# Kernel tuning notes

Hardware: AMD Instinct MI355X
Metric: run time of the kernel (lower is better)

## Reference

```python
import jax, jax.numpy as jnp
import numpy as np

T, C, NH, NL, NP = 5, 192, 4, 5, 4
DH = C // NH

def leaky(x):
    return jnp.where(x >= 0, x, 0.1 * x)

def conv2d(x, w, b, padding=1, dilation=1):
    out = jax.lax.conv_general_dilated(
        x, w, window_strides=(1, 1),
        padding=[(padding, padding), (padding, padding)],
        rhs_dilation=(dilation, dilation),
        dimension_numbers=('NCHW', 'OIHW', 'NCHW'))
    return out + b[None, :, None, None]

def grid_sample_border(img, gx, gy):
    # align_corners=True, padding_mode='border'; gx/gy normalized [-1,1], shape (B,H,W)
    B, Cc, H, W = img.shape
    x = jnp.clip((gx + 1.0) * 0.5 * (W - 1), 0.0, W - 1)
    y = jnp.clip((gy + 1.0) * 0.5 * (H - 1), 0.0, H - 1)
    x0 = jnp.floor(x); y0 = jnp.floor(y)
    wx = (x - x0).reshape(B, 1, -1); wy = (y - y0).reshape(B, 1, -1)
    flat = img.reshape(B, Cc, H * W)
    def g(yi, xi):
        xi = jnp.clip(xi, 0, W - 1).astype(jnp.int32)
        yi = jnp.clip(yi, 0, H - 1).astype(jnp.int32)
        return jnp.take_along_axis(flat, (yi * W + xi).reshape(B, 1, -1), axis=2)
    out = (g(y0, x0) * (1 - wx) * (1 - wy) + g(y0, x0 + 1) * wx * (1 - wy)
         + g(y0 + 1, x0) * (1 - wx) * wy + g(y0 + 1, x0 + 1) * wx * wy)
    return out.reshape(B, Cc, H, W)

def warp(x, flo):
    B, _, H, W = x.shape
    xx = jnp.arange(W, dtype=jnp.float32)[None, :] * jnp.ones((H, 1), jnp.float32)
    yy = jnp.arange(H, dtype=jnp.float32)[:, None] * jnp.ones((1, W), jnp.float32)
    gx = 2.0 * (xx[None] + flo[:, 0]) / max(W - 1, 1) - 1.0
    gy = 2.0 * (yy[None] + flo[:, 1]) / max(H - 1, 1) - 1.0
    return grid_sample_border(x, gx, gy)

def deform_sample(v_img, loc):
    # v_img (N,D,H,W); loc (N,Q,P,2) in [0,1]; bilinear, zeros padding, align_corners=False
    N, D, H, W = v_img.shape
    Q, P = loc.shape[1], loc.shape[2]
    x = loc[..., 0] * W - 0.5
    y = loc[..., 1] * H - 0.5
    x0 = jnp.floor(x); y0 = jnp.floor(y)
    wx = (x - x0).reshape(N, 1, -1); wy = (y - y0).reshape(N, 1, -1)
    flat = v_img.reshape(N, D, H * W)
    def g(yi, xi):
        valid = ((xi >= 0) & (xi <= W - 1) & (yi >= 0) & (yi <= H - 1)).astype(v_img.dtype)
        xi_c = jnp.clip(xi, 0, W - 1).astype(jnp.int32)
        yi_c = jnp.clip(yi, 0, H - 1).astype(jnp.int32)
        return jnp.take_along_axis(flat, (yi_c * W + xi_c).reshape(N, 1, -1), axis=2) * valid.reshape(N, 1, -1)
    out = (g(y0, x0) * (1 - wx) * (1 - wy) + g(y0, x0 + 1) * wx * (1 - wy)
         + g(y0 + 1, x0) * (1 - wx) * wy + g(y0 + 1, x0 + 1) * wx * wy)
    return out.reshape(N, D, Q, P)

def _forward(frame, srcframe, flow_forward, flow_backward,
             w_qk, b_qk, w_v, b_v, w_vproj, b_vproj, w_off, b_off,
             w_attn, b_attn, w_out, b_out, w_ff, b_ff,
             w_ffn1, b_ffn1, w_ffn2, b_ffn2):
    b, t, c, h, w = frame.shape
    ff01, ff12 = flow_forward[:, 0], flow_forward[:, 1]
    fb32, fb43 = flow_backward[:, 2], flow_backward[:, 3]
    ff02 = ff01 + warp(ff12, ff01)
    fb42 = fb43 + warp(fb32, fb43)
    warp02 = warp(frame[:, 0], ff02)
    warp12 = warp(frame[:, 1], ff12)
    warp32 = warp(frame[:, 3], fb32)
    warp42 = warp(frame[:, 4], fb42)
    qk_in = jnp.concatenate([warp02, warp12, frame[:, 2], warp32, warp42,
                             flow_forward.reshape(b, -1, h, w),
                             flow_backward.reshape(b, -1, h, w)], axis=1)
    queries = leaky(conv2d(qk_in, w_qk, b_qk)).reshape(b, t, c, h, w)
    value = leaky(conv2d(frame.reshape(b, t * c, h, w), w_v, b_v)).reshape(b, t, c, h, w)

    Lq = t * h * w
    q_tok = queries.transpose(0, 1, 3, 4, 2).reshape(b, Lq, c)
    v_tok = value.transpose(0, 1, 3, 4, 2).reshape(b, Lq, c)
    v_proj = (v_tok @ w_vproj.T + b_vproj).reshape(b, t, h * w, NH, DH)

    offs = (q_tok @ w_off.T + b_off).reshape(b, Lq, NH, NL, NP, 2)
    aw = (q_tok @ w_attn.T + b_attn).reshape(b, Lq, NH, NL * NP)
    aw = jax.nn.softmax(aw, axis=-1).reshape(b, Lq, NH, NL, NP)

    # reference points (all valid ratios are ones): ((x+0.5)/W, (y+0.5)/H)
    rx = (jnp.arange(w, dtype=frame.dtype) + 0.5) / w
    ry = (jnp.arange(h, dtype=frame.dtype) + 0.5) / h
    ref = jnp.stack(jnp.meshgrid(rx, ry, indexing='xy'), axis=-1).reshape(h * w, 2)
    ref = jnp.tile(ref, (t, 1))  # (Lq, 2)

    norm = jnp.array([w, h], dtype=frame.dtype)
    # flow-guided per-level displacement toward the center frame (level 2)
    zero = jnp.zeros_like(ff12)
    flows = jnp.stack([ff02, ff12, zero, fb32, fb42], axis=1)  # (b,NL,2,h,w)
    flow_norm = (flows / norm[None, None, :, None, None]).transpose(0, 1, 3, 4, 2).reshape(b, NL, h * w, 2)
    flow_norm = jnp.tile(flow_norm.transpose(0, 2, 1, 3), (1, t, 1, 1))  # (b,Lq,NL,2)

    loc = (ref[None, :, None, None, None, :]
           + offs / norm[None, None, None, None, None, :]
           + flow_norm[:, :, None, :, None, :])  # (b,Lq,NH,NL,NP,2)

    acc = jnp.zeros((b * NH, DH, Lq), dtype=frame.dtype)
    for l in range(NL):
        v_l = v_proj[:, l].transpose(0, 2, 3, 1).reshape(b * NH, DH, h, w)
        loc_l = loc[:, :, :, l].transpose(0, 2, 1, 3, 4).reshape(b * NH, Lq, NP, 2)
        samp = deform_sample(v_l, loc_l)  # (b*NH, DH, Lq, NP)
        w_l = aw[:, :, :, l].transpose(0, 2, 1, 3).reshape(b * NH, 1, Lq, NP)
        acc = acc + (samp * w_l).sum(-1)
    attn = acc.reshape(b, NH, DH, Lq).transpose(0, 3, 1, 2).reshape(b, Lq, c)
    attn = attn @ w_out.T + b_out

    out = attn.reshape(b, t, h, w, c).transpose(0, 1, 4, 2, 3).reshape(b * t, c, h, w)
    out = conv2d(out, w_ff, b_ff)
    out = out.reshape(b, t, c, h, w) + frame
    seq_in = jnp.concatenate([out.reshape(b * t, c, h, w), srcframe.reshape(b * t, c, h, w)], axis=1)
    ffn = conv2d(seq_in, w_ffn1, b_ffn1, padding=2, dilation=2)
    ffn = conv2d(leaky(ffn), w_ffn2, b_ffn2)
    out = out.reshape(b * t, c, h, w) + ffn
    return out.reshape(b, t, c, h, w)

def setup_inputs():
    key = jax.random.key(0)
    ks = jax.random.split(key, 16)
    B, H, W = 2, 64, 64
    s = 0.02
    d = {}
    d['frame'] = jax.random.normal(ks[0], (B, T, C, H, W), jnp.float32)
    d['srcframe'] = jax.random.normal(ks[1], (B, T, C, H, W), jnp.float32)
    d['flow_forward'] = jax.random.normal(ks[2], (B, 4, 2, H, W), jnp.float32)
    d['flow_backward'] = jax.random.normal(ks[3], (B, 4, 2, H, W), jnp.float32)
    cin_qk = T * C + 4 * (T - 1)
    d['w_qk'] = jax.random.normal(ks[4], (T * C, cin_qk, 3, 3), jnp.float32) * s
    d['b_qk'] = jnp.zeros((T * C,), jnp.float32)
    d['w_v'] = jax.random.normal(ks[5], (T * C, T * C, 3, 3), jnp.float32) * s
    d['b_v'] = jnp.zeros((T * C,), jnp.float32)
    d['w_vproj'] = jax.random.normal(ks[6], (C, C), jnp.float32) * s
    d['b_vproj'] = jnp.zeros((C,), jnp.float32)
    d['w_off'] = jax.random.normal(ks[7], (NH * NL * NP * 2, C), jnp.float32) * s
    d['b_off'] = jax.random.normal(ks[8], (NH * NL * NP * 2,), jnp.float32)
    d['w_attn'] = jax.random.normal(ks[9], (NH * NL * NP, C), jnp.float32) * s
    d['b_attn'] = jnp.zeros((NH * NL * NP,), jnp.float32)
    d['w_out'] = jax.random.normal(ks[10], (C, C), jnp.float32) * s
    d['b_out'] = jnp.zeros((C,), jnp.float32)
    d['w_ff'] = jax.random.normal(ks[11], (C, C, 3, 3), jnp.float32) * s
    d['b_ff'] = jnp.zeros((C,), jnp.float32)
    d['w_ffn1'] = jax.random.normal(ks[12], (C, 2 * C, 3, 3), jnp.float32) * s
    d['b_ffn1'] = jnp.zeros((C,), jnp.float32)
    d['w_ffn2'] = jax.random.normal(ks[13], (C, C, 3, 3), jnp.float32) * s
    d['b_ffn2'] = jnp.zeros((C,), jnp.float32)
    return d

def reference(frame, srcframe, flow_forward, flow_backward, w_qk, b_qk, w_v, b_v, w_vproj, b_vproj, w_off, b_off, w_attn, b_attn, w_out, b_out, w_ff, b_ff, w_ffn1, b_ffn1, w_ffn2, b_ffn2):
    out = _forward(frame, srcframe, flow_forward, flow_backward, w_qk, b_qk, w_v, b_v, w_vproj, b_vproj, w_off, b_off, w_attn, b_attn, w_out, b_out, w_ff, b_ff, w_ffn1, b_ffn1, w_ffn2, b_ffn2)
    return (out, srcframe)
```

## Files before the change

### kernel.cpp

```cpp
#include <hip/hip_runtime.h>


#define HWPX 4096
#define PPXN 4624
#define LQ   20480

typedef __attribute__((ext_vector_type(8))) short  short8;
typedef __attribute__((ext_vector_type(4))) short  short4v;
typedef __attribute__((ext_vector_type(4))) float  f32x4;

__device__ __forceinline__ unsigned short f2bf(float f) {
    unsigned u = __float_as_uint(f);
    unsigned r = (u + 0x7FFF + ((u >> 16) & 1)) >> 16;
    return (unsigned short)r;
}
__device__ __forceinline__ float bf2f(unsigned short s) {
    return __uint_as_float(((unsigned)s) << 16);
}

__device__ __forceinline__ void gl_lds16(const unsigned short* g, unsigned short* l) {
    __builtin_amdgcn_global_load_lds(
        (const __attribute__((address_space(1))) unsigned int*)g,
        (__attribute__((address_space(3))) unsigned int*)l, 16, 0, 0);
}

__device__ __forceinline__ float bsample(const float* __restrict__ p, float sx, float sy) {
    sx = fminf(fmaxf(sx, 0.f), 63.f);
    sy = fminf(fmaxf(sy, 0.f), 63.f);
    float x0 = floorf(sx), y0 = floorf(sy);
    int ix0 = (int)x0, iy0 = (int)y0;
    int ix1 = ix0 < 63 ? ix0 + 1 : 63;
    int iy1 = iy0 < 63 ? iy0 + 1 : 63;
    float wx = sx - x0, wy = sy - y0;
    float v00 = p[iy0*64+ix0], v01 = p[iy0*64+ix1];
    float v10 = p[iy1*64+ix0], v11 = p[iy1*64+ix1];
    return (v00*(1.f-wx) + v01*wx)*(1.f-wy) + (v10*(1.f-wx) + v11*wx)*wy;
}

__device__ void dev_flow(int i, const float* __restrict__ ff,
                         const float* __restrict__ fb, float* __restrict__ flows) {
    int b = i >> 12, pix = i & 4095;
    int x = pix & 63, y = pix >> 6;
    const float* ff01 = ff + (size_t)(b*4+0)*2*HWPX;
    const float* ff12 = ff + (size_t)(b*4+1)*2*HWPX;
    const float* fb32 = fb + (size_t)(b*4+2)*2*HWPX;
    const float* fb43 = fb + (size_t)(b*4+3)*2*HWPX;
    float* F = flows + (size_t)b*5*2*HWPX;
    float ax = ff01[pix], ay = ff01[HWPX+pix];
    float sx = bsample(ff12,      (float)x+ax, (float)y+ay);
    float sy = bsample(ff12+HWPX, (float)x+ax, (float)y+ay);
    F[0*2*HWPX + pix]        = ax + sx;
    F[0*2*HWPX + HWPX + pix] = ay + sy;
    F[1*2*HWPX + pix]        = ff12[pix];
    F[1*2*HWPX + HWPX + pix] = ff12[HWPX+pix];
    F[2*2*HWPX + pix]        = 0.f;
    F[2*2*HWPX + HWPX + pix] = 0.f;
    F[3*2*HWPX + pix]        = fb32[pix];
    F[3*2*HWPX + HWPX + pix] = fb32[HWPX+pix];
    float bx = fb43[pix], by = fb43[HWPX+pix];
    float tx = bsample(fb32,      (float)x+bx, (float)y+by);
    float ty = bsample(fb32+HWPX, (float)x+bx, (float)y+by);
    F[4*2*HWPX + pix]        = bx + tx;
    F[4*2*HWPX + HWPX + pix] = by + ty;
}

__device__ void dev_wT(const float* __restrict__ w, unsigned short* __restrict__ wT,
                       int CI, int NKB, int cotile, int kblk, int tid) {
    unsigned short* dst = wT + ((size_t)(cotile*NKB + kblk))*18432;
    #pragma unroll
    for (int it = 0; it < 9; ++it) {
        int idx = it*256 + tid;
        int tap = idx >> 8, sub = idx & 255;
        int cg = sub >> 6, co = sub & 63;
        int cog = cotile*64 + co;
        int ci0 = kblk*32 + cg*8;
        short8 v;
        #pragma unroll
        for (int j = 0; j < 8; ++j) {
            int ci = ci0 + j;
            v[j] = (ci < CI) ? (short)f2bf(w[((size_t)cog*CI + ci)*9 + tap]) : (short)0;
        }
        *(short8*)(dst + (size_t)idx*8) = v;
    }
}

__device__ void dev_wg(const float* __restrict__ w1, const float* __restrict__ w2,
                       unsigned short* __restrict__ wg, int co_split, int CO,
                       int cotile, int tid) {
    unsigned short* dst = wg + (size_t)cotile*12288;
    #pragma unroll
    for (int it = 0; it < 6; ++it) {
        int idx = it*256 + tid;
        int kblk = idx >> 8, sub = idx & 255;
        int cg = sub >> 6, co = sub & 63;
        int cog = cotile*64 + co;
        int ci0 = kblk*32 + cg*8;
        short8 v = {};
        if (cog < CO) {
            const float* row = (cog < co_split) ? w1 + (size_t)cog*192
                                                : w2 + (size_t)(cog - co_split)*192;
            #pragma unroll
            for (int j = 0; j < 8; ++j) v[j] = (short)f2bf(row[ci0 + j]);
        }
        *(short8*)(dst + (size_t)idx*8) = v;
    }
}

__global__ __launch_bounds__(256) void k_wprep(
    const float* __restrict__ flow_f, const float* __restrict__ flow_b,
    float* __restrict__ flows,
    const float* __restrict__ w_qk, unsigned short* __restrict__ wT_qk,
    const float* __restrict__ w_v,  unsigned short* __restrict__ wT_v,
    const float* __restrict__ w_ff, unsigned short* __restrict__ wT_ff,
    const float* __restrict__ w_f1, unsigned short* __restrict__ wT_f1,
    const float* __restrict__ w_f2, unsigned short* __restrict__ wT_f2,
    const float* __restrict__ w_vp, const float* __restrict__ w_off,
    const float* __restrict__ w_at, const float* __restrict__ w_out,
    unsigned short* __restrict__ wg_vp, unsigned short* __restrict__ wg_oa,
    unsigned short* __restrict__ wg_out)
{
    int bid = blockIdx.x, tid = threadIdx.x;
    if (bid < 32) {
        dev_flow(bid*256 + tid, flow_f, flow_b, flows);
    } else if (bid < 497) {
        int p = bid - 32;   dev_wT(w_qk, wT_qk, 976, 31, p/31, p%31, tid);
    } else if (bid < 947) {
        int p = bid - 497;  dev_wT(w_v,  wT_v,  960, 30, p/30, p%30, tid);
    } else if (bid < 965) {
        int p = bid - 947;  dev_wT(w_ff, wT_ff, 192, 6,  p/6,  p%6,  tid);
    } else if (bid < 1001) {
        int p = bid - 965;  dev_wT(w_f1, wT_f1, 384, 12, p/12, p%12, tid);
    } else if (bid < 1019) {
        int p = bid - 1001; dev_wT(w_f2, wT_f2, 192, 6,  p/6,  p%6,  tid);
    } else {
        int g = bid - 1019;
        if (g < 3)      dev_wg(w_vp,  nullptr, wg_vp, 192, 192, g,   tid);
        else if (g < 7) dev_wg(w_off, w_at,    wg_oa, 160, 240, g-3, tid);
        else            dev_wg(w_out, nullptr, wg_out, 192, 192, g-7, tid);
    }
}

__global__ void k_qkin(const unsigned short* __restrict__ Pv,
                       const float* __restrict__ ff, const float* __restrict__ fb,
                       const float* __restrict__ flows,
                       unsigned short* __restrict__ Pqk)
{
    int ppx = blockIdx.x*64 + threadIdx.x;
    if (ppx >= PPXN) return;
    int b = blockIdx.z;
    int c8 = (blockIdx.y*4 + threadIdx.y)*8;
    unsigned short* dst = Pqk + ((size_t)b*PPXN + ppx)*992 + c8;
    int py = ppx/68, pxc = ppx - py*68;
    short8 o = {};
    if (py >= 2 && py < 66 && pxc >= 2 && pxc < 66 && c8 < 976) {
        int y = py-2, x = pxc-2, pix = (y<<6)+x;
        if (c8 >= 960) {
            #pragma unroll
            for (int j = 0; j < 8; ++j) {
                int k = c8 - 960 + j;
                float v = (k < 8) ? ff[((size_t)b*8 + k)*HWPX + pix]
                                  : fb[((size_t)b*8 + k - 8)*HWPX + pix];
                o[j] = (short)f2bf(v);
            }
        } else {
            const unsigned short* Pvb = Pv + (size_t)b*PPXN*960;
            int slot = c8/192;
            if (slot == 2) {
                o = *(const short8*)(Pvb + (size_t)ppx*960 + c8);
            } else {
                const float* F = flows + ((size_t)(b*5 + slot)*2)*HWPX;
                float sx = fminf(fmaxf((float)x + F[pix], 0.f), 63.f);
                float sy = fminf(fmaxf((float)y + F[HWPX + pix], 0.f), 63.f);
                float x0 = floorf(sx), y0 = floorf(sy);
                int ix0 = (int)x0, iy0 = (int)y0;
                int ix1 = ix0 < 63 ? ix0+1 : 63, iy1 = iy0 < 63 ? iy0+1 : 63;
                float wx = sx - x0, wy = sy - y0;
                float w00 = (1.f-wx)*(1.f-wy), w01 = wx*(1.f-wy);
                float w10 = (1.f-wx)*wy,       w11 = wx*wy;
                short8 v00 = *(const short8*)(Pvb + ((size_t)((iy0+2)*68 + ix0+2))*960 + c8);
                short8 v01 = *(const short8*)(Pvb + ((size_t)((iy0+2)*68 + ix1+2))*960 + c8);
                short8 v10 = *(const short8*)(Pvb + ((size_t)((iy1+2)*68 + ix0+2))*960 + c8);
                short8 v11 = *(const short8*)(Pvb + ((size_t)((iy1+2)*68 + ix1+2))*960 + c8);
                #pragma unroll
                for (int j = 0; j < 8; ++j) {
                    float v = bf2f((unsigned short)v00[j])*w00 + bf2f((unsigned short)v01[j])*w01
                            + bf2f((unsigned short)v10[j])*w10 + bf2f((unsigned short)v11[j])*w11;
                    o[j] = (short)f2bf(v);
                }
            }
        }
    }
    *(short8*)dst = o;
}

__global__ void t_pad(const float* __restrict__ in, unsigned short* __restrict__ outb,
                      int CI, int PITCH, int COFF)
{
    int ppx = blockIdx.x*64 + threadIdx.x;
    if (ppx >= PPXN) return;
    int img = blockIdx.z;
    int c8 = (blockIdx.y*4 + threadIdx.y)*8;
    unsigned short* dst = outb + ((size_t)img*PPXN + ppx)*PITCH;
    int py = ppx/68, pxc = ppx - py*68;
    if (py < 2 || py >= 66 || pxc < 2 || pxc >= 66) {
        short8 z = {};
        *(short8*)(dst + c8) = z;
        if (COFF) *(short8*)(dst + COFF + c8) = z;
        return;
    }
    int pix = ((py-2)<<6) + (pxc-2);
    short8 o;
    #pragma unroll
    for (int j = 0; j < 8; ++j)
        o[j] = (short)f2bf(in[((size_t)img*CI + c8 + j)*HWPX + pix]);
    *(short8*)(dst + COFF + c8) = o;
}

__global__ __launch_bounds__(256) void t_zb(unsigned short* __restrict__ b0,
                                            unsigned short* __restrict__ b1) {
    int id = blockIdx.x*256 + threadIdx.x;
    int ppx = id / 24, c8 = (id - ppx*24) * 8;
    if (ppx >= PPXN) return;
    int py = ppx/68, pxc = ppx - py*68;
    if (py >= 2 && py < 66 && pxc >= 2 && pxc < 66) return;
    int y = blockIdx.y;
    unsigned short* buf = (y < 10) ? b0 : b1;
    int img = (y < 10) ? y : y - 10;
    short8 z = {};
    *(short8*)(buf + ((size_t)img*PPXN + ppx)*192 + c8) = z;
}

template<int ROWS, int DIL, int OUTK, bool LEAKY, int RESK>
__global__ __launch_bounds__(256, 2) void k_conv(
    const unsigned short* __restrict__ P0, const unsigned short* __restrict__ P1,
    int CIP0, int CIP1, int NKB0, int NKB1,
    const unsigned short* __restrict__ wT0, const unsigned short* __restrict__ wT1,
    const float* __restrict__ bias0, const float* __restrict__ bias1,
    const float* __restrict__ resF, const unsigned short* __restrict__ resB, int resPitch,
    float* __restrict__ outF,
    unsigned short* __restrict__ outB0, unsigned short* __restrict__ outB1,
    int outPitch, int outCoff, int njobs)
{
    constexpr int RR     = ROWS*4 + 2*DIL;
    constexpr int XP     = 64 + 2*DIL;
    constexpr int PLANE  = RR*XP*16;
    constexpr int NCH    = RR*XP*4;
    constexpr int NXS    = (NCH + 255)/256;
    constexpr int TILEPX = ROWS*4*64;
    constexpr int SMEM_K = 4*PLANE + 36864;
    constexpr int SMEM_E = (OUTK <= 1) ? TILEPX*72*2 : 0;
    constexpr int SMEMSZ = SMEM_K > SMEM_E ? SMEM_K : SMEM_E;
    __shared__ __align__(16) unsigned char smem[SMEMSZ];
    unsigned char*  s_x = smem;
    unsigned short* s_w = (unsigned short*)(smem + 4*PLANE);

    int tid = threadIdx.x & 255;
    int gx = gridDim.x, gy = gridDim.y, gz = gridDim.z;
    int lin = blockIdx.x + gx*(blockIdx.y + gy*blockIdx.z);
    int tot = gx*gy*gz;
    if ((tot & 7) == 0) { int q = tot >> 3; lin = (lin & 7)*q + (lin >> 3); }
    int cotile = lin % gx; int rem = lin / gx;
    int ytile = rem % gy;  int z = rem / gy;

    int sel = (njobs == 2) ? (z >> 1) : 0;
    int img = (njobs == 2) ? (z & 1)  : z;
    const unsigned short* P  = sel ? P1  : P0;
    const unsigned short* wT = sel ? wT1 : wT0;
    const float* bias        = sel ? bias1 : bias0;
    unsigned short* outB     = sel ? outB1 : outB0;
    int CIP = sel ? CIP1 : CIP0;
    int NKB = sel ? NKB1 : NKB0;

    int y0 = ytile * (ROWS*4);
    const unsigned short* Pi = P + (size_t)img*PPXN*CIP;
    int w = tid >> 6, lane = tid & 63, lm = lane & 15, cig = lane >> 4;

    auto stage_x = [&](int kb) {
        int k0 = kb*32;
        #pragma unroll
        for (int it = 0; it < NXS; ++it) {
            int li = it*256 + tid;
            if (li < NCH) {
                int p = li / (RR*XP), rm = li - p*(RR*XP);
                int r = rm / XP, c = rm - r*XP;
                gl_lds16(Pi + ((size_t)((y0 + 2 - DIL + r)*68 + c + 2 - DIL))*CIP + k0 + p*8,
                         (unsigned short*)(s_x + li*16));
            }
        }
    };
    auto stage_w = [&](int kb) {
        const unsigned short* ws = wT + ((size_t)(cotile*NKB + kb))*18432;
        #pragma unroll
        for (int it = 0; it < 9; ++it)
            gl_lds16(ws + (size_t)(it*256+tid)*8, &s_w[(it*256+tid)*8]);
    };

    stage_x(0); stage_w(0);
    __syncthreads();

    f32x4 acc[4][ROWS*4] = {};
    for (int kb = 0; kb < NKB; ++kb) {
        __builtin_amdgcn_s_setprio(1);
        #pragma unroll
        for (int t = 0; t < 9; ++t) {
            int ky = t/3, kx = t - ky*3;
            short8 A[4];
            #pragma unroll
            for (int mb = 0; mb < 4; ++mb)
                A[mb] = *(const short8*)&s_w[((t*4 + cig)*64 + mb*16 + lm)*8];
            #pragma unroll
            for (int s = 0; s < ROWS; ++s) {
                short8 Bf[4];
                #pragma unroll
                for (int nc = 0; nc < 4; ++nc)
                    Bf[nc] = *(const short8*)&s_x[cig*PLANE +
                               ((w*ROWS + s + ky*DIL)*XP + nc*16 + lm + kx*DIL)*16];
                #pragma unroll
                for (int mb = 0; mb < 4; ++mb)
                    #pragma unroll
                    for (int nc = 0; nc < 4; ++nc)
                        acc[mb][s*4+nc] = __builtin_amdgcn_mfma_f32_16x16x32_bf16(
                            A[mb], Bf[nc], acc[mb][s*4+nc], 0, 0, 0);
            }
        }
        __builtin_amdgcn_s_setprio(0);
        __syncthreads();
        if (kb + 1 < NKB) { stage_x(kb+1); stage_w(kb+1); }
        __syncthreads();
    }

    if (OUTK == 0 || OUTK == 1) {
        unsigned short* epi = (unsigned short*)smem;
        #pragma unroll
        for (int mb = 0; mb < 4; ++mb) {
            int cob = cotile*64 + mb*16 + cig*4;
            int col = mb*16 + cig*4;
            #pragma unroll
            for (int s = 0; s < ROWS; ++s) {
                int lr = w*ROWS + s;
                #pragma unroll
                for (int nc = 0; nc < 4; ++nc) {
                    int x = nc*16 + lm;
                    int px_l = lr*64 + x;
                    int gpx = y0*64 + px_l;
                    short4v sv;
                    #pragma unroll
                    for (int r = 0; r < 4; ++r) {
                        float v = acc[mb][s*4+nc][r] + bias[cob + r];
                        if (LEAKY) v = v >= 0.f ? v : 0.1f*v;
                        if (RESK == 1) v += resF[((size_t)img*192 + cob + r)*HWPX + gpx];
                        sv[r] = (short)f2bf(v);
                    }
                    *(short4v*)&epi[px_l*72 + col] = sv;
                }
            }
        }
        __syncthreads();
        constexpr int NCPY = TILEPX/32;
        int slot = (OUTK == 0) ? (cotile*64)/192 : 0;
        int ccb  = (OUTK == 0) ? (cotile*64)%192 : (cotile*64 + outCoff);
        #pragma unroll
        for (int it2 = 0; it2 < NCPY; ++it2) {
            int li = it2*256 + tid;
            int px_l = li >> 3, sub = li & 7;
            short8 v = *(const short8*)&epi[px_l*72 + sub*8];
            int gpx = y0*64 + px_l;
            if (OUTK == 0) {
                *(short8*)(outB + ((size_t)(img*5 + slot)*HWPX + gpx)*192 + ccb + sub*8) = v;
            } else {
                int ppx = ((gpx>>6)+2)*68 + (gpx&63) + 2;
                *(short8*)(outB0 + ((size_t)img*PPXN + ppx)*outPitch + ccb + sub*8) = v;
            }
        }
    } else {
        #pragma unroll
        for (int mb = 0; mb < 4; ++mb) {
            int cob = cotile*64 + mb*16 + cig*4;
            #pragma unroll
            for (int s = 0; s < ROWS; ++s) {
                int y = y0 + w*ROWS + s;
                #pragma unroll
                for (int nc = 0; nc < 4; ++nc) {
                    int x = nc*16 + lm;
                    int px = (y<<6) + x;
                    int ppx = (y+2)*68 + x + 2;
                    short4v rv;
                    if (RESK == 2)
                        rv = *(const short4v*)(resB + ((size_t)img*PPXN + ppx)*resPitch + cob);
                    #pragma unroll
                    for (int r = 0; r < 4; ++r) {
                        float v = acc[mb][s*4+nc][r] + bias[cob + r];
                        if (LEAKY) v = v >= 0.f ? v : 0.1f*v;
                        if (RESK == 1) v += resF[((size_t)img*192 + cob + r)*HWPX + px];
                        if (RESK == 2) v += bf2f((unsigned short)rv[r]);
                        outF[((size_t)img*192 + cob + r)*HWPX + px] = v;
                    }
                }
            }
        }
    }
}

template<int GMODE>
__global__ __launch_bounds__(256) void k_gemmm(
    const unsigned short* __restrict__ X, const unsigned short* __restrict__ WG,
    const float* __restrict__ b1, const float* __restrict__ b2,
    float* __restrict__ o1, float* __restrict__ o2, unsigned short* __restrict__ ob)
{
    __shared__ unsigned char  s_x[2][4*4096];
    __shared__ unsigned short s_w[12288];
    int tid = threadIdx.x & 255;
    int cotile = blockIdx.x, pxt = blockIdx.y, img = blockIdx.z;
    int px0 = pxt*256;
    const unsigned short* Xi = X + (size_t)img*HWPX*192;
    #pragma unroll
    for (int it = 0; it < 6; ++it)
        gl_lds16(WG + (size_t)cotile*12288 + (it*256+tid)*8, &s_w[(it*256+tid)*8]);
    short8 xr[4];
    #pragma unroll
    for (int it = 0; it < 4; ++it)
        xr[it] = *(const short8*)(Xi + (size_t)(px0 + tid)*192 + it*8);
    #pragma unroll
    for (int it = 0; it < 4; ++it)
        *(short8*)&s_x[0][it*4096 + tid*16] = xr[it];
    __syncthreads();
    int w = tid >> 6, lane = tid & 63, lm = lane & 15, cig = lane >> 4;
    f32x4 acc[4][4] = {};
    int xb = 0;
    for (int kb = 0; kb < 6; ++kb) {
        bool pf = (kb < 5);
        if (pf) {
            int k0 = (kb+1)*32;
            #pragma unroll
            for (int it = 0; it < 4; ++it)
                xr[it] = *(const short8*)(Xi + (size_t)(px0 + tid)*192 + k0 + it*8);
        }
        short8 A[4], Bf[4];
        #pragma unroll
        for (int nb = 0; nb < 4; ++nb)
            Bf[nb] = *(const short8*)&s_x[xb][cig*4096 + (w*64 + nb*16 + lm)*16];
        #pragma unroll
        for (int mb = 0; mb < 4; ++mb)
            A[mb] = *(const short8*)&s_w[((kb*4 + cig)*64 + mb*16 + lm)*8];
        #pragma unroll
        for (int mb = 0; mb < 4; ++mb)
            #pragma unroll
            for (int nb = 0; nb < 4; ++nb)
                acc[mb][nb] = __builtin_amdgcn_mfma_f32_16x16x32_bf16(
                    A[mb], Bf[nb], acc[mb][nb], 0, 0, 0);
        if (pf) {
            #pragma unroll
            for (int it = 0; it < 4; ++it)
                *(short8*)&s_x[xb^1][it*4096 + tid*16] = xr[it];
        }
        __syncthreads();
        xb ^= 1;
    }
    int b = img/5, t = img - b*5;
    #pragma unroll
    for (int mb = 0; mb < 4; ++mb) {
        int cob = cotile*64 + mb*16 + cig*4;
        if (GMODE == 1 && cob >= 240) continue;
        #pragma unroll
        for (int nb = 0; nb < 4; ++nb) {
            int px = px0 + w*64 + nb*16 + lm;
            float vv[4];
            #pragma unroll
            for (int r = 0; r < 4; ++r) {
                float bv;
                if (GMODE == 1) bv = (cob + r < 160) ? b1[cob+r] : b2[cob+r-160];
                else bv = b1[cob + r];
                vv[r] = acc[mb][nb][r] + bv;
            }
            if (GMODE == 0) {
                int h = cob/48, d = cob - h*48;
                short4v s;
                #pragma unroll
                for (int r = 0; r < 4; ++r) s[r] = (short)f2bf(vv[r]);
                *(short4v*)(ob + (((size_t)img*4 + h)*HWPX + px)*48 + d) = s;
            } else if (GMODE == 1) {
                #pragma unroll
                for (int r = 0; r < 4; ++r) {
                    int co = cob + r;
                    if (co < 160) o1[((size_t)b*160 + co)*LQ + t*HWPX + px] = vv[r];
                    else          o2[((size_t)b*80 + co-160)*LQ + t*HWPX + px] = vv[r];
                }
            } else {
                int ppx = ((px>>6)+2)*68 + (px&63) + 2;
                short4v s;
                #pragma unroll
                for (int r = 0; r < 4; ++r) s[r] = (short)f2bf(vv[r]);
                *(short4v*)(ob + ((size_t)img*PPXN + ppx)*192 + cob) = s;
            }
        }
    }
}

__device__ __forceinline__ void addtap(float* acc, const unsigned short* __restrict__ src, float w) {
    const short8* s8 = (const short8*)src;
    #pragma unroll
    for (int q = 0; q < 6; ++q) {
        short8 v = s8[q];
        #pragma unroll
        for (int j = 0; j < 8; ++j)
            acc[q*8+j] += w * bf2f((unsigned short)v[j]);
    }
}

__global__ __launch_bounds__(256) void k_sample(
    const unsigned short* __restrict__ vp, const float* __restrict__ offs,
    const float* __restrict__ aw, const float* __restrict__ flows,
    unsigned short* __restrict__ accout)
{
    int blk = blockIdx.x;
    int b = blk / 320, sub = blk - b*320;
    int h = threadIdx.x >> 6;
    int lq = sub*64 + (threadIdx.x & 63);
    int pix = lq & 4095;
    int x = pix & 63, y = pix >> 6;
    const float* offp = offs + ((size_t)b*160 + h*40)*LQ + lq;
    const float* awp  = aw   + ((size_t)b*80  + h*20)*LQ + lq;
    float e[20];
    float m = -1e30f;
    #pragma unroll
    for (int j = 0; j < 20; ++j) { e[j] = awp[(size_t)j*LQ]; m = fmaxf(m, e[j]); }
    float ssum = 0.f;
    #pragma unroll
    for (int j = 0; j < 20; ++j) { e[j] = __expf(e[j]-m); ssum += e[j]; }
    float inv = 1.f/ssum;

    float acc[48];
    #pragma unroll
    for (int d = 0; d < 48; ++d) acc[d] = 0.f;

    for (int l = 0; l < 5; ++l) {
        float fx = flows[((size_t)(b*5+l)*2+0)*HWPX + pix];
        float fy = flows[((size_t)(b*5+l)*2+1)*HWPX + pix];
        const unsigned short* vpl = vp + ((size_t)(b*5+l)*4 + h)*HWPX*48;
        #pragma unroll
        for (int p = 0; p < 4; ++p) {
            int o = l*4 + p;
            float ox = offp[(size_t)(2*o)*LQ];
            float oy = offp[(size_t)(2*o+1)*LQ];
            float wv = e[o]*inv;
            float sx = (float)x + ox + fx;
            float sy = (float)y + oy + fy;
            float x0f = floorf(sx), y0f = floorf(sy);
            float wx = sx - x0f, wy = sy - y0f;
            int ix0 = (int)x0f, iy0 = (int)y0f;
            float w00 = wv*(1.f-wx)*(1.f-wy), w01 = wv*wx*(1.f-wy);
            float w10 = wv*(1.f-wx)*wy,       w11 = wv*wx*wy;
            bool vx0 = (ix0 >= 0)  && (ix0 <= 63);
            bool vx1 = (ix0 >= -1) && (ix0 <= 62);
            bool vy0 = (iy0 >= 0)  && (iy0 <= 63);
            bool vy1 = (iy0 >= -1) && (iy0 <= 62);
            if (vy0 && vx0) addtap(acc, vpl + (size_t)(iy0*64 + ix0)*48,       w00);
            if (vy0 && vx1) addtap(acc, vpl + (size_t)(iy0*64 + ix0 + 1)*48,   w01);
            if (vy1 && vx0) addtap(acc, vpl + (size_t)((iy0+1)*64 + ix0)*48,   w10);
            if (vy1 && vx1) addtap(acc, vpl + (size_t)((iy0+1)*64 + ix0+1)*48, w11);
        }
    }
    unsigned short* dst = accout + ((size_t)b*LQ + lq)*192 + h*48;
    #pragma unroll
    for (int q = 0; q < 6; ++q) {
        short8 s;
        #pragma unroll
        for (int j = 0; j < 8; ++j) s[j] = (short)f2bf(acc[q*8+j]);
        *(short8*)(dst + q*8) = s;
    }
}


extern "C" void kernel_launch(void* const* d_in, const int* in_sizes, int n_in,
                              void* d_out, int out_size, void* d_ws, size_t ws_size,
                              hipStream_t stream) {
    (void)in_sizes; (void)n_in; (void)out_size; (void)ws_size;
    const float* frame    = (const float*)d_in[0];
    const float* srcframe = (const float*)d_in[1];
    const float* flow_f   = (const float*)d_in[2];
    const float* flow_b   = (const float*)d_in[3];
    const float* w_qk  = (const float*)d_in[4];  const float* b_qk  = (const float*)d_in[5];
    const float* w_v   = (const float*)d_in[6];  const float* b_v   = (const float*)d_in[7];
    const float* w_vp  = (const float*)d_in[8];  const float* b_vp  = (const float*)d_in[9];
    const float* w_off = (const float*)d_in[10]; const float* b_off = (const float*)d_in[11];
    const float* w_at  = (const float*)d_in[12]; const float* b_at  = (const float*)d_in[13];
    const float* w_out = (const float*)d_in[14]; const float* b_out = (const float*)d_in[15];
    const float* w_ff  = (const float*)d_in[16]; const float* b_ff  = (const float*)d_in[17];
    const float* w_f1  = (const float*)d_in[18]; const float* b_f1  = (const float*)d_in[19];
    const float* w_f2  = (const float*)d_in[20]; const float* b_f2  = (const float*)d_in[21];
    float* out = (float*)d_out;
    char* W = (char*)d_ws;

    float*          flows  = (float*)(W + 0);
    unsigned short* wT_qk  = (unsigned short*)(W + 327680);
    unsigned short* wT_v   = (unsigned short*)(W + 17469440);
    unsigned short* P_qk   = (unsigned short*)(W + 34058240);
    unsigned short* P_ff   = P_qk;
    unsigned short* P_v    = (unsigned short*)(W + 52406272);
    unsigned short* P_mid  = P_v;
    unsigned short* Q_tok  = (unsigned short*)(W + 70162432);
    unsigned short* acc_tok= Q_tok;
    unsigned short* V_tok  = (unsigned short*)(W + 85891072);
    unsigned short* P_ffn1 = V_tok;
    unsigned short* vp     = (unsigned short*)(W + 101619712);
    float*          offs   = (float*)(W + 121403392);
    float*          aw     = (float*)(W + 147617792);
    unsigned short* wT_ff  = (unsigned short*)(W + 160724992);
    unsigned short* wT_f1  = (unsigned short*)(W + 161388544);
    unsigned short* wT_f2  = (unsigned short*)(W + 162715648);
    unsigned short* wg_vp  = (unsigned short*)(W + 163379200);
    unsigned short* wg_oa  = (unsigned short*)(W + 163452928);
    unsigned short* wg_out = (unsigned short*)(W + 163551232);

    dim3 bp(64, 4);

    k_wprep<<<1029, 256, 0, stream>>>(
        flow_f, flow_b, flows,
        w_qk, wT_qk, w_v, wT_v, w_ff, wT_ff, w_f1, wT_f1, w_f2, wT_f2,
        w_vp, w_off, w_at, w_out, wg_vp, wg_oa, wg_out);
    t_pad<<<dim3(73,30,2), bp, 0, stream>>>(frame, P_v, 960, 960, 0);
    k_qkin<<<dim3(73,31,2), bp, 0, stream>>>(P_v, flow_f, flow_b, flows, P_qk);
    k_conv<2,1,0,true,0><<<dim3(15,8,4), 256, 0, stream>>>(
        P_qk, P_v, 992, 960, 31, 30, wT_qk, wT_v, b_qk, b_v,
        nullptr, nullptr, 0, nullptr, Q_tok, V_tok, 0, 0, 2);
    t_zb<<<dim3(434,20), 256, 0, stream>>>(P_ff, P_mid);
    k_gemmm<0><<<dim3(3,16,10), 256, 0, stream>>>(V_tok, wg_vp, b_vp, nullptr,
                                                  nullptr, nullptr, vp);
    k_gemmm<1><<<dim3(4,16,10), 256, 0, stream>>>(Q_tok, wg_oa, b_off, b_at,
                                                  offs, aw, nullptr);
    k_sample<<<640, 256, 0, stream>>>(vp, offs, aw, flows, acc_tok);
    t_pad<<<dim3(73,6,10), bp, 0, stream>>>(srcframe, P_ffn1, 192, 384, 192);
    k_gemmm<2><<<dim3(3,16,10), 256, 0, stream>>>(acc_tok, wg_out, b_out, nullptr,
                                                  nullptr, nullptr, P_ff);
    k_conv<1,1,1,false,1><<<dim3(3,16,10), 256, 0, stream>>>(
        P_ff, nullptr, 192, 0, 6, 0, wT_ff, nullptr, b_ff, nullptr,
        frame, nullptr, 0, nullptr, P_ffn1, nullptr, 384, 0, 1);
    k_conv<1,2,1,true,0><<<dim3(3,16,10), 256, 0, stream>>>(
        P_ffn1, nullptr, 384, 0, 12, 0, wT_f1, nullptr, b_f1, nullptr,
        nullptr, nullptr, 0, nullptr, P_mid, nullptr, 192, 0, 1);
    k_conv<1,1,2,false,2><<<dim3(3,16,10), 256, 0, stream>>>(
        P_mid, nullptr, 192, 0, 6, 0, wT_f2, nullptr, b_f2, nullptr,
        nullptr, P_ffn1, 384, out, nullptr, nullptr, 0, 0, 1);
    hipMemcpyAsync(out + (size_t)2*5*192*HWPX, srcframe,
                   (size_t)2*5*192*HWPX*sizeof(float),
                   hipMemcpyDeviceToDevice, stream);
}
```

Before: 955.6 us.

## Merge small kernels into fewer launches and change value-projection layout

Several launches are folded together. The srcframe-to-output copy moves into the weight-prep kernel. The two token GEMMs and the border zeroing share one launch. The output GEMM and the srcframe padding share another, and the separate memcpy is removed. The value-projection output is now stored pixel-major with all heads contiguous (pitch 192), and the sampler is updated to match. The intent is to cut launch overhead and idle tails between small kernels. In exchange, branchy merged kernels can have uneven block workloads, and the new vp layout changes the sampler's gather stride.

```diff
diff --git a/kernel.cpp b/kernel.cpp
--- a/kernel.cpp
+++ b/kernel.cpp
@@ -8,6 +8,7 @@
 typedef __attribute__((ext_vector_type(8))) short  short8;
 typedef __attribute__((ext_vector_type(4))) short  short4v;
 typedef __attribute__((ext_vector_type(4))) float  f32x4;
+typedef __attribute__((ext_vector_type(4))) float  float4v;
 
 __device__ __forceinline__ unsigned short f2bf(float f) {
     unsigned u = __float_as_uint(f);
@@ -106,6 +107,27 @@
     }
 }
 
+__device__ void dev_pad(const float* __restrict__ in, unsigned short* __restrict__ outb,
+                        int CI, int PITCH, int COFF, int img, int ppx_t, int cq, int tid) {
+    int ppx = ppx_t*64 + (tid & 63);
+    if (ppx >= PPXN) return;
+    int c8 = (cq*4 + (tid >> 6))*8;
+    unsigned short* dst = outb + ((size_t)img*PPXN + ppx)*PITCH;
+    int py = ppx/68, pxc = ppx - py*68;
+    if (py < 2 || py >= 66 || pxc < 2 || pxc >= 66) {
+        short8 z = {};
+        *(short8*)(dst + c8) = z;
+        if (COFF) *(short8*)(dst + COFF + c8) = z;
+        return;
+    }
+    int pix = ((py-2)<<6) + (pxc-2);
+    short8 o;
+    #pragma unroll
+    for (int j = 0; j < 8; ++j)
+        o[j] = (short)f2bf(in[((size_t)img*CI + c8 + j)*HWPX + pix]);
+    *(short8*)(dst + COFF + c8) = o;
+}
+
 __global__ __launch_bounds__(256) void k_wprep(
     const float* __restrict__ flow_f, const float* __restrict__ flow_b,
     float* __restrict__ flows,
@@ -117,7 +139,8 @@
     const float* __restrict__ w_vp, const float* __restrict__ w_off,
     const float* __restrict__ w_at, const float* __restrict__ w_out,
     unsigned short* __restrict__ wg_vp, unsigned short* __restrict__ wg_oa,
-    unsigned short* __restrict__ wg_out)
+    unsigned short* __restrict__ wg_out,
+    const float* __restrict__ srcframe, float* __restrict__ out2)
 {
     int bid = blockIdx.x, tid = threadIdx.x;
     if (bid < 32) {
@@ -132,11 +155,20 @@
         int p = bid - 965;  dev_wT(w_f1, wT_f1, 384, 12, p/12, p%12, tid);
     } else if (bid < 1019) {
         int p = bid - 1001; dev_wT(w_f2, wT_f2, 192, 6,  p/6,  p%6,  tid);
-    } else {
+    } else if (bid < 1029) {
         int g = bid - 1019;
         if (g < 3)      dev_wg(w_vp,  nullptr, wg_vp, 192, 192, g,   tid);
         else if (g < 7) dev_wg(w_off, w_at,    wg_oa, 160, 240, g-3, tid);
         else            dev_wg(w_out, nullptr, wg_out, 192, 192, g-7, tid);
+    } else {
+        int c = bid - 1029;
+        const float4v* s4 = (const float4v*)srcframe;
+        float4v* d4 = (float4v*)out2;
+        #pragma unroll
+        for (int it = 0; it < 8; ++it) {
+            int idx = it*245760 + c*256 + tid;
+            d4[idx] = s4[idx];
+        }
     }
 }
 
@@ -216,20 +248,6 @@
     *(short8*)(dst + COFF + c8) = o;
 }
 
-__global__ __launch_bounds__(256) void t_zb(unsigned short* __restrict__ b0,
-                                            unsigned short* __restrict__ b1) {
-    int id = blockIdx.x*256 + threadIdx.x;
-    int ppx = id / 24, c8 = (id - ppx*24) * 8;
-    if (ppx >= PPXN) return;
-    int py = ppx/68, pxc = ppx - py*68;
-    if (py >= 2 && py < 66 && pxc >= 2 && pxc < 66) return;
-    int y = blockIdx.y;
-    unsigned short* buf = (y < 10) ? b0 : b1;
-    int img = (y < 10) ? y : y - 10;
-    short8 z = {};
-    *(short8*)(buf + ((size_t)img*PPXN + ppx)*192 + c8) = z;
-}
-
 template<int ROWS, int DIL, int OUTK, bool LEAKY, int RESK>
 __global__ __launch_bounds__(256, 2) void k_conv(
     const unsigned short* __restrict__ P0, const unsigned short* __restrict__ P1,
@@ -401,98 +419,155 @@
     }
 }
 
-template<int GMODE>
-__global__ __launch_bounds__(256) void k_gemmm(
-    const unsigned short* __restrict__ X, const unsigned short* __restrict__ WG,
-    const float* __restrict__ b1, const float* __restrict__ b2,
-    float* __restrict__ o1, float* __restrict__ o2, unsigned short* __restrict__ ob)
+#define GEMM_CORE(Xi, WG_, cotile_)                                              \
+    _Pragma("unroll")                                                            \
+    for (int it = 0; it < 6; ++it)                                               \
+        gl_lds16(WG_ + (size_t)(cotile_)*12288 + (it*256+tid)*8,                 \
+                 &s_w[(it*256+tid)*8]);                                          \
+    short8 xr[4];                                                                \
+    _Pragma("unroll")                                                            \
+    for (int it = 0; it < 4; ++it)                                               \
+        xr[it] = *(const short8*)(Xi + (size_t)(px0 + tid)*192 + it*8);          \
+    _Pragma("unroll")                                                            \
+    for (int it = 0; it < 4; ++it)                                               \
+        *(short8*)&s_x[0][it*4096 + tid*16] = xr[it];                            \
+    __syncthreads();                                                             \
+    int w = tid >> 6, lane = tid & 63, lm = lane & 15, cig = lane >> 4;          \
+    f32x4 acc[4][4] = {};                                                        \
+    int xb = 0;                                                                  \
+    for (int kb = 0; kb < 6; ++kb) {                                             \
+        bool pf = (kb < 5);                                                      \
+        if (pf) {                                                                \
+            int k0 = (kb+1)*32;                                                  \
+            _Pragma("unroll")                                                    \
+            for (int it = 0; it < 4; ++it)                                       \
+                xr[it] = *(const short8*)(Xi + (size_t)(px0 + tid)*192 + k0 + it*8); \
+        }                                                                        \
+        short8 A[4], Bf[4];                                                      \
+        _Pragma("unroll")                                                        \
+        for (int nb = 0; nb < 4; ++nb)                                           \
+            Bf[nb] = *(const short8*)&s_x[xb][cig*4096 + (w*64 + nb*16 + lm)*16];\
+        _Pragma("unroll")                                                        \
+        for (int mb = 0; mb < 4; ++mb)                                           \
+            A[mb] = *(const short8*)&s_w[((kb*4 + cig)*64 + mb*16 + lm)*8];      \
+        _Pragma("unroll")                                                        \
+        for (int mb = 0; mb < 4; ++mb)                                           \
+            _Pragma("unroll")                                                    \
+            for (int nb = 0; nb < 4; ++nb)                                       \
+                acc[mb][nb] = __builtin_amdgcn_mfma_f32_16x16x32_bf16(           \
+                    A[mb], Bf[nb], acc[mb][nb], 0, 0, 0);                        \
+        if (pf) {                                                                \
+            _Pragma("unroll")                                                    \
+            for (int it = 0; it < 4; ++it)                                       \
+                *(short8*)&s_x[xb^1][it*4096 + tid*16] = xr[it];                 \
+        }                                                                        \
+        __syncthreads();                                                         \
+        xb ^= 1;                                                                 \
+    }
+
+__global__ __launch_bounds__(256) void k_gemmA(
+    const unsigned short* __restrict__ Xv, const unsigned short* __restrict__ WGv,
+    const float* __restrict__ bvp, unsigned short* __restrict__ vp,
+    const unsigned short* __restrict__ Xq, const unsigned short* __restrict__ WGq,
+    const float* __restrict__ boff, const float* __restrict__ batt,
+    float* __restrict__ offs, float* __restrict__ aw,
+    unsigned short* __restrict__ P_ff, unsigned short* __restrict__ P_mid)
 {
     __shared__ unsigned char  s_x[2][4*4096];
     __shared__ unsigned short s_w[12288];
     int tid = threadIdx.x & 255;
-    int cotile = blockIdx.x, pxt = blockIdx.y, img = blockIdx.z;
-    int px0 = pxt*256;
-    const unsigned short* Xi = X + (size_t)img*HWPX*192;
-    #pragma unroll
-    for (int it = 0; it < 6; ++it)
-        gl_lds16(WG + (size_t)cotile*12288 + (it*256+tid)*8, &s_w[(it*256+tid)*8]);
-    short8 xr[4];
-    #pragma unroll
-    for (int it = 0; it < 4; ++it)
-        xr[it] = *(const short8*)(Xi + (size_t)(px0 + tid)*192 + it*8);
-    #pragma unroll
-    for (int it = 0; it < 4; ++it)
-        *(short8*)&s_x[0][it*4096 + tid*16] = xr[it];
-    __syncthreads();
-    int w = tid >> 6, lane = tid & 63, lm = lane & 15, cig = lane >> 4;
-    f32x4 acc[4][4] = {};
-    int xb = 0;
-    for (int kb = 0; kb < 6; ++kb) {
-        bool pf = (kb < 5);
-        if (pf) {
-            int k0 = (kb+1)*32;
-            #pragma unroll
-            for (int it = 0; it < 4; ++it)
-                xr[it] = *(const short8*)(Xi + (size_t)(px0 + tid)*192 + k0 + it*8);
-        }
-        short8 A[4], Bf[4];
-        #pragma unroll
-        for (int nb = 0; nb < 4; ++nb)
-            Bf[nb] = *(const short8*)&s_x[xb][cig*4096 + (w*64 + nb*16 + lm)*16];
-        #pragma unroll
-        for (int mb = 0; mb < 4; ++mb)
-            A[mb] = *(const short8*)&s_w[((kb*4 + cig)*64 + mb*16 + lm)*8];
-        #pragma unroll
-        for (int mb = 0; mb < 4; ++mb)
-            #pragma unroll
-            for (int nb = 0; nb < 4; ++nb)
-                acc[mb][nb] = __builtin_amdgcn_mfma_f32_16x16x32_bf16(
-                    A[mb], Bf[nb], acc[mb][nb], 0, 0, 0);
-        if (pf) {
-            #pragma unroll
-            for (int it = 0; it < 4; ++it)
-                *(short8*)&s_x[xb^1][it*4096 + tid*16] = xr[it];
-        }
-        __syncthreads();
-        xb ^= 1;
-    }
-    int b = img/5, t = img - b*5;
-    #pragma unroll
-    for (int mb = 0; mb < 4; ++mb) {
-        int cob = cotile*64 + mb*16 + cig*4;
-        if (GMODE == 1 && cob >= 240) continue;
-        #pragma unroll
-        for (int nb = 0; nb < 4; ++nb) {
-            int px = px0 + w*64 + nb*16 + lm;
-            float vv[4];
-            #pragma unroll
-            for (int r = 0; r < 4; ++r) {
-                float bv;
-                if (GMODE == 1) bv = (cob + r < 160) ? b1[cob+r] : b2[cob+r-160];
-                else bv = b1[cob + r];
-                vv[r] = acc[mb][nb][r] + bv;
-            }
-            if (GMODE == 0) {
-                int h = cob/48, d = cob - h*48;
+    int id = blockIdx.x;
+    if (id < 480) {
+        int cotile = id % 3, pxt = (id/3) % 16, img = id/48;
+        int px0 = pxt*256;
+        const unsigned short* Xi = Xv + (size_t)img*HWPX*192;
+        GEMM_CORE(Xi, WGv, cotile)
+        #pragma unroll
+        for (int mb = 0; mb < 4; ++mb) {
+            int cob = cotile*64 + mb*16 + cig*4;
+            #pragma unroll
+            for (int nb = 0; nb < 4; ++nb) {
+                int px = px0 + w*64 + nb*16 + lm;
                 short4v s;
                 #pragma unroll
-                for (int r = 0; r < 4; ++r) s[r] = (short)f2bf(vv[r]);
-                *(short4v*)(ob + (((size_t)img*4 + h)*HWPX + px)*48 + d) = s;
-            } else if (GMODE == 1) {
+                for (int r = 0; r < 4; ++r)
+                    s[r] = (short)f2bf(acc[mb][nb][r] + bvp[cob + r]);
+                *(short4v*)(vp + ((size_t)img*HWPX + px)*192 + cob) = s;
+            }
+        }
+    } else if (id < 1120) {
+        int i2 = id - 480;
+        int cotile = i2 % 4, pxt = (i2/4) % 16, img = i2/64;
+        int px0 = pxt*256;
+        const unsigned short* Xi = Xq + (size_t)img*HWPX*192;
+        GEMM_CORE(Xi, WGq, cotile)
+        int b = img/5, t = img - b*5;
+        #pragma unroll
+        for (int mb = 0; mb < 4; ++mb) {
+            int cob = cotile*64 + mb*16 + cig*4;
+            if (cob >= 240) continue;
+            #pragma unroll
+            for (int nb = 0; nb < 4; ++nb) {
+                int px = px0 + w*64 + nb*16 + lm;
                 #pragma unroll
                 for (int r = 0; r < 4; ++r) {
                     int co = cob + r;
-                    if (co < 160) o1[((size_t)b*160 + co)*LQ + t*HWPX + px] = vv[r];
-                    else          o2[((size_t)b*80 + co-160)*LQ + t*HWPX + px] = vv[r];
+                    float bv = (co < 160) ? boff[co] : batt[co-160];
+                    float v = acc[mb][nb][r] + bv;
+                    if (co < 160) offs[((size_t)b*160 + co)*LQ + t*HWPX + px] = v;
+                    else          aw[((size_t)b*80 + co-160)*LQ + t*HWPX + px] = v;
                 }
-            } else {
+            }
+        }
+    } else {
+        int u = (id - 1120)*256 + tid;
+        int c8i = u % 24; int r1 = u / 24;
+        int b = r1 % 528; int r2 = r1 / 528;
+        int img = r2 % 10; int buf = r2 / 10;
+        int ppx;
+        if (b < 136) ppx = b;
+        else if (b < 272) ppx = 4488 + (b - 136);
+        else { int b2 = b - 272; int row = 2 + (b2 >> 2); int cs = b2 & 3;
+               ppx = row*68 + ((cs < 2) ? cs : cs + 64); }
+        unsigned short* bp2 = buf ? P_mid : P_ff;
+        short8 z = {};
+        *(short8*)(bp2 + ((size_t)img*PPXN + ppx)*192 + c8i*8) = z;
+    }
+}
+
+__global__ __launch_bounds__(256) void k_tailB(
+    const unsigned short* __restrict__ X, const unsigned short* __restrict__ WG,
+    const float* __restrict__ b1, unsigned short* __restrict__ P_ff,
+    const float* __restrict__ srcframe, unsigned short* __restrict__ P_ffn1)
+{
+    __shared__ unsigned char  s_x[2][4*4096];
+    __shared__ unsigned short s_w[12288];
+    int tid = threadIdx.x & 255;
+    int id = blockIdx.x;
+    if (id < 480) {
+        int cotile = id % 3, pxt = (id/3) % 16, img = id/48;
+        int px0 = pxt*256;
+        const unsigned short* Xi = X + (size_t)img*HWPX*192;
+        GEMM_CORE(Xi, WG, cotile)
+        #pragma unroll
+        for (int mb = 0; mb < 4; ++mb) {
+            int cob = cotile*64 + mb*16 + cig*4;
+            #pragma unroll
+            for (int nb = 0; nb < 4; ++nb) {
+                int px = px0 + w*64 + nb*16 + lm;
                 int ppx = ((px>>6)+2)*68 + (px&63) + 2;
                 short4v s;
                 #pragma unroll
-                for (int r = 0; r < 4; ++r) s[r] = (short)f2bf(vv[r]);
-                *(short4v*)(ob + ((size_t)img*PPXN + ppx)*192 + cob) = s;
-            }
-        }
+                for (int r = 0; r < 4; ++r)
+                    s[r] = (short)f2bf(acc[mb][nb][r] + b1[cob + r]);
+                *(short4v*)(P_ff + ((size_t)img*PPXN + ppx)*192 + cob) = s;
+            }
+        }
+    } else {
+        int p = id - 480;
+        int img = p / 438, rem = p - img*438;
+        int ppx_t = rem % 73, cq = rem / 73;
+        dev_pad(srcframe, P_ffn1, 192, 384, 192, img, ppx_t, cq, tid);
     }
 }
 
@@ -536,7 +611,7 @@
     for (int l = 0; l < 5; ++l) {
         float fx = flows[((size_t)(b*5+l)*2+0)*HWPX + pix];
         float fy = flows[((size_t)(b*5+l)*2+1)*HWPX + pix];
-        const unsigned short* vpl = vp + ((size_t)(b*5+l)*4 + h)*HWPX*48;
+        const unsigned short* vpl = vp + ((size_t)(b*5+l)*HWPX)*192 + h*48;
         #pragma unroll
         for (int p = 0; p < 4; ++p) {
             int o = l*4 + p;
@@ -554,10 +629,10 @@
             bool vx1 = (ix0 >= -1) && (ix0 <= 62);
             bool vy0 = (iy0 >= 0)  && (iy0 <= 63);
             bool vy1 = (iy0 >= -1) && (iy0 <= 62);
-            if (vy0 && vx0) addtap(acc, vpl + (size_t)(iy0*64 + ix0)*48,       w00);
-            if (vy0 && vx1) addtap(acc, vpl + (size_t)(iy0*64 + ix0 + 1)*48,   w01);
-            if (vy1 && vx0) addtap(acc, vpl + (size_t)((iy0+1)*64 + ix0)*48,   w10);
-            if (vy1 && vx1) addtap(acc, vpl + (size_t)((iy0+1)*64 + ix0+1)*48, w11);
+            if (vy0 && vx0) addtap(acc, vpl + (size_t)(iy0*64 + ix0)*192,       w00);
+            if (vy0 && vx1) addtap(acc, vpl + (size_t)(iy0*64 + ix0 + 1)*192,   w01);
+            if (vy1 && vx0) addtap(acc, vpl + (size_t)((iy0+1)*64 + ix0)*192,   w10);
+            if (vy1 && vx1) addtap(acc, vpl + (size_t)((iy0+1)*64 + ix0+1)*192, w11);
         }
     }
     unsigned short* dst = accout + ((size_t)b*LQ + lq)*192 + h*48;
@@ -614,24 +689,21 @@
 
     dim3 bp(64, 4);
 
-    k_wprep<<<1029, 256, 0, stream>>>(
+    k_wprep<<<1989, 256, 0, stream>>>(
         flow_f, flow_b, flows,
         w_qk, wT_qk, w_v, wT_v, w_ff, wT_ff, w_f1, wT_f1, w_f2, wT_f2,
-        w_vp, w_off, w_at, w_out, wg_vp, wg_oa, wg_out);
+        w_vp, w_off, w_at, w_out, wg_vp, wg_oa, wg_out,
+        srcframe, out + (size_t)2*5*192*HWPX);
     t_pad<<<dim3(73,30,2), bp, 0, stream>>>(frame, P_v, 960, 960, 0);
     k_qkin<<<dim3(73,31,2), bp, 0, stream>>>(P_v, flow_f, flow_b, flows, P_qk);
     k_conv<2,1,0,true,0><<<dim3(15,8,4), 256, 0, stream>>>(
         P_qk, P_v, 992, 960, 31, 30, wT_qk, wT_v, b_qk, b_v,
         nullptr, nullptr, 0, nullptr, Q_tok, V_tok, 0, 0, 2);
-    t_zb<<<dim3(434,20), 256, 0, stream>>>(P_ff, P_mid);
-    k_gemmm<0><<<dim3(3,16,10), 256, 0, stream>>>(V_tok, wg_vp, b_vp, nullptr,
-                                                  nullptr, nullptr, vp);
-    k_gemmm<1><<<dim3(4,16,10), 256, 0, stream>>>(Q_tok, wg_oa, b_off, b_at,
-                                                  offs, aw, nullptr);
+    k_gemmA<<<2110, 256, 0, stream>>>(
+        V_tok, wg_vp, b_vp, vp, Q_tok, wg_oa, b_off, b_at, offs, aw, P_ff, P_mid);
     k_sample<<<640, 256, 0, stream>>>(vp, offs, aw, flows, acc_tok);
-    t_pad<<<dim3(73,6,10), bp, 0, stream>>>(srcframe, P_ffn1, 192, 384, 192);
-    k_gemmm<2><<<dim3(3,16,10), 256, 0, stream>>>(acc_tok, wg_out, b_out, nullptr,
-                                                  nullptr, nullptr, P_ff);
+    k_tailB<<<4860, 256, 0, stream>>>(acc_tok, wg_out, b_out, P_ff,
+                                      srcframe, P_ffn1);
     k_conv<1,1,1,false,1><<<dim3(3,16,10), 256, 0, stream>>>(
         P_ff, nullptr, 192, 0, 6, 0, wT_ff, nullptr, b_ff, nullptr,
         frame, nullptr, 0, nullptr, P_ffn1, nullptr, 384, 0, 1);
@@ -641,7 +713,4 @@
     k_conv<1,1,2,false,2><<<dim3(3,16,10), 256, 0, stream>>>(
         P_mid, nullptr, 192, 0, 6, 0, wT_f2, nullptr, b_f2, nullptr,
         nullptr, P_ffn1, 384, out, nullptr, nullptr, 0, 0, 1);
-    hipMemcpyAsync(out + (size_t)2*5*192*HWPX, srcframe,
-                   (size_t)2*5*192*HWPX*sizeof(float),
-                   hipMemcpyDeviceToDevice, stream);
-}
+}
```

Result: no change. 966.7 us (+1.2%).
